# Optimization experiments

Measured on AMD Instinct MI355X. Metric: run time of the kernel, lower is better.

## Reference

```python
import jax, jax.numpy as jnp
import numpy as np

T, D_MODEL = 2048, 6144
NH, NKV, HD = 48, 8, 128
THETA, CAP = 10000.0, 30.0


def setup_inputs() -> dict:
    key = jax.random.key(0)
    k1, k2, k3 = jax.random.split(key, 3)
    return {
        "positions": jnp.arange(T, dtype=jnp.int32),
        "hidden_states": jax.random.normal(k1, (T, D_MODEL), jnp.float32),
        "w_qkv": jax.random.normal(k2, (D_MODEL, (NH + 2 * NKV) * HD), jnp.float32) * 0.02,
        "w_o": jax.random.normal(k3, (NH * HD, D_MODEL), jnp.float32) * 0.02,
    }


def _rope_neox(positions, x):
    # x: [T, h, HD]; neox-style: rotate concatenated halves
    half = HD // 2
    inv_freq = 1.0 / (THETA ** (jnp.arange(0, HD, 2, dtype=jnp.float32) / HD))  # [half]
    freqs = positions.astype(jnp.float32)[:, None] * inv_freq  # [T, half]
    cos = jnp.cos(freqs)[:, None, :]  # [T,1,half]
    sin = jnp.sin(freqs)[:, None, :]
    x1, x2 = x[..., :half], x[..., half:]
    return jnp.concatenate([x1 * cos - x2 * sin, x2 * cos + x1 * sin], axis=-1)


def reference(positions, hidden_states, w_qkv, w_o):
    qkv = hidden_states @ w_qkv  # [T, (NH+2*NKV)*HD]
    q, k, v = jnp.split(qkv, [NH * HD, NH * HD + NKV * HD], axis=-1)
    q = q.reshape(T, NH, HD)
    k = k.reshape(T, NKV, HD)
    v = v.reshape(T, NKV, HD)
    q = _rope_neox(positions, q)
    k = _rope_neox(positions, k)
    # GQA: expand kv heads to query heads
    g = NH // NKV
    k = jnp.repeat(k, g, axis=1)  # [T, NH, HD]
    v = jnp.repeat(v, g, axis=1)
    scale = HD ** -0.5
    logits = jnp.einsum('thd,shd->hts', q, k) * scale  # [NH, T, T]
    logits = CAP * jnp.tanh(logits / CAP)  # tanh logit softcapping
    causal = positions[:, None] >= positions[None, :]  # [T, T]
    logits = jnp.where(causal[None, :, :], logits, -jnp.inf)
    probs = jax.nn.softmax(logits, axis=-1)
    out = jnp.einsum('hts,shd->thd', probs, v)  # [T, NH, HD]
    out = out.reshape(T, NH * HD)
    return out @ w_o
```

## Files before the change

### kernel.cpp

```cpp
#include <hip/hip_runtime.h>
#include <hip/hip_bf16.h>
#include <stdint.h>

#define TSEQ   2048
#define DMODEL 6144
#define NHEADS 48
#define NKVH   8
#define HDIM   128
#define QKVC   8192
#define GRP    6

typedef __attribute__((ext_vector_type(8))) short short8;
typedef __attribute__((ext_vector_type(4))) float f32x4;


__device__ __forceinline__ unsigned short f2b(float f) {
  union { float f; unsigned int u; } v; v.f = f;
  unsigned int u = v.u;
  unsigned int r = (u + 0x7FFFu + ((u >> 16) & 1u)) >> 16;
  return (unsigned short)r;
}

__device__ __forceinline__ float b2f(unsigned short s) {
  union { unsigned int u; float f; } v; v.u = ((unsigned int)s) << 16;
  return v.f;
}

#if __has_builtin(__builtin_amdgcn_exp2f)
#define EXP2(x) __builtin_amdgcn_exp2f(x)
#else
#define EXP2(x) exp2f(x)
#endif
#if __has_builtin(__builtin_amdgcn_rcpf)
#define RCP(x) __builtin_amdgcn_rcpf(x)
#else
#define RCP(x) (1.0f / (x))
#endif

typedef const __attribute__((address_space(1))) void* as1_cvp;
typedef __attribute__((address_space(3))) void* as3_vp;

__device__ __forceinline__ void gload_lds16(const void* g, void* l) {
  __builtin_amdgcn_global_load_lds(
      (as1_cvp)(uintptr_t)g,
      (as3_vp)(unsigned int)(uintptr_t)l, 16, 0, 0);
}

#define LGKMC(n) do { asm volatile("s_waitcnt lgkmcnt(" #n ")" ::: "memory"); \
                      __builtin_amdgcn_sched_barrier(0); } while (0)
#define VMC(n) do { asm volatile("s_waitcnt vmcnt(" #n ")" ::: "memory"); \
                    __builtin_amdgcn_sched_barrier(0); } while (0)
#define BARR  do { asm volatile("s_barrier" ::: "memory"); } while (0)


__global__ __launch_bounds__(256) void k_cvt(const float* __restrict__ in,
                                             unsigned short* __restrict__ outp, int n) {
  int i = (blockIdx.x * 256 + threadIdx.x) * 8;
  if (i + 7 < n) {
    float4 va = *(const float4*)(in + i);
    float4 vb = *(const float4*)(in + i + 4);
    union { unsigned short s[8]; uint4 u; } o;
    o.s[0] = f2b(va.x); o.s[1] = f2b(va.y); o.s[2] = f2b(va.z); o.s[3] = f2b(va.w);
    o.s[4] = f2b(vb.x); o.s[5] = f2b(vb.y); o.s[6] = f2b(vb.z); o.s[7] = f2b(vb.w);
    *(uint4*)(outp + i) = o.u;
  }
}

__global__ __launch_bounds__(256) void k_tr2(const float* __restrict__ in, long istr, long zin,
                                             unsigned short* __restrict__ out, long ostr, long zout) {
  __shared__ unsigned short tile[64][68];
  const int tid = threadIdx.x;
  const int br = blockIdx.y * 64;
  const int bc = blockIdx.x * 64;
  in  += (size_t)blockIdx.z * zin;
  out += (size_t)blockIdx.z * zout;
  const int row = tid >> 4;
  const int c4  = (tid & 15) * 4;
#pragma unroll
  for (int p = 0; p < 4; ++p) {
    const int r = p * 16 + row;
    float4 v = *(const float4*)(in + (size_t)(br + r) * istr + bc + c4);
    tile[r][c4 + 0] = f2b(v.x);
    tile[r][c4 + 1] = f2b(v.y);
    tile[r][c4 + 2] = f2b(v.z);
    tile[r][c4 + 3] = f2b(v.w);
  }
  __syncthreads();
#pragma unroll
  for (int p = 0; p < 4; ++p) {
    const int r = p * 16 + row;
    union { unsigned short s[4]; uint2 u; } o;
    o.s[0] = tile[c4 + 0][r];
    o.s[1] = tile[c4 + 1][r];
    o.s[2] = tile[c4 + 2][r];
    o.s[3] = tile[c4 + 3][r];
    *(uint2*)(out + (size_t)(bc + r) * ostr + br + c4) = o.u;
  }
}

__global__ __launch_bounds__(256) void k_tr2b(const unsigned short* __restrict__ in, long istr, long zin,
                                              unsigned short* __restrict__ out, long ostr, long zout) {
  __shared__ unsigned short tile[64][68];
  const int tid = threadIdx.x;
  const int br = blockIdx.y * 64;
  const int bc = blockIdx.x * 64;
  in  += (size_t)blockIdx.z * zin;
  out += (size_t)blockIdx.z * zout;
  const int row = tid >> 4;
  const int c4  = (tid & 15) * 4;
#pragma unroll
  for (int p = 0; p < 4; ++p) {
    const int r = p * 16 + row;
    union { unsigned short s[4]; uint2 u; } v;
    v.u = *(const uint2*)(in + (size_t)(br + r) * istr + bc + c4);
    tile[r][c4 + 0] = v.s[0];
    tile[r][c4 + 1] = v.s[1];
    tile[r][c4 + 2] = v.s[2];
    tile[r][c4 + 3] = v.s[3];
  }
  __syncthreads();
#pragma unroll
  for (int p = 0; p < 4; ++p) {
    const int r = p * 16 + row;
    union { unsigned short s[4]; uint2 u; } o;
    o.s[0] = tile[c4 + 0][r];
    o.s[1] = tile[c4 + 1][r];
    o.s[2] = tile[c4 + 2][r];
    o.s[3] = tile[c4 + 3][r];
    *(uint2*)(out + (size_t)(bc + r) * ostr + br + c4) = o.u;
  }
}

__global__ void k_trig(const int* __restrict__ pos, float* __restrict__ cs,
                       float* __restrict__ sn) {
  int t = blockIdx.x, i = threadIdx.x;
  float p = (float)pos[t];
  float inv = EXP2(-(float)(2 * i) * (1.0f / 128.0f) * 13.287712379549449f);
  float f = p * inv;
  cs[t * 64 + i] = cosf(f);
  sn[t * 64 + i] = sinf(f);
}


#define READ_A(mh, aa) do { \
  _Pragma("unroll") for (int m = 0; m < 4; ++m) \
  _Pragma("unroll") for (int ks = 0; ks < 2; ++ks) \
    aa[m][ks] = *(const short8*)(LA + (wm * 128 + (mh) * 64 + m * 16 + lr) * 128 \
                                 + ((ks * 64 + lkb) ^ lsw)); } while (0)

#define READ_BR(s, cnt, bb) do { \
  _Pragma("unroll") for (int n2 = (s); n2 < (s) + (cnt); ++n2) \
  _Pragma("unroll") for (int ks = 0; ks < 2; ++ks) \
    bb[n2][ks] = *(const short8*)(LB + (wn * (16 * NH2) + n2 * 16 + lr) * 128 \
                                  + ((ks * 64 + lkb) ^ lsw)); } while (0)

#define CLUSTER(mh, s, cnt, aa, bb) do { \
  __builtin_amdgcn_s_setprio(1); \
  _Pragma("unroll") for (int m = 0; m < 4; ++m) \
  _Pragma("unroll") for (int n2 = (s); n2 < (s) + (cnt); ++n2) \
  _Pragma("unroll") for (int ks = 0; ks < 2; ++ks) \
    acc[(mh) * 4 + m][n2] = __builtin_amdgcn_mfma_f32_16x16x32_bf16( \
        aa[m][ks], bb[n2][ks], acc[(mh) * 4 + m][n2], 0, 0, 0); \
  __builtin_amdgcn_s_setprio(0); } while (0)

#define STAGE_A(kt, bb) do { \
  _Pragma("unroll") for (int i = 0; i < 4; ++i) \
    gload_lds16(Asrc + (size_t)(kt) * 64 + (size_t)i * 64 * K, \
                lds + (bb) * BUFSZ + F + i * 8192); } while (0)

#define STAGE_B(kt, bb) do { \
  _Pragma("unroll") for (int i = 0; i < NH2; ++i) \
    gload_lds16(Bsrc + (size_t)(kt) * 64 + (size_t)i * 64 * K, \
                lds + (bb) * BUFSZ + 32768 + F + i * 8192); } while (0)

template <int NH2, typename OutT>
__global__ __launch_bounds__(512, 2) void k_gemm8(const unsigned short* __restrict__ A,
                                                  const unsigned short* __restrict__ Bt,
                                                  OutT* __restrict__ C,
                                                  int M, int N, int K) {
  extern __shared__ __align__(16) unsigned char lds[];
  constexpr int BN    = 64 * NH2;
  constexpr int NB0   = (NH2 == 4) ? 2 : 1;
  constexpr int NB1   = NH2 - NB0;
  constexpr int BUFSZ = 32768 + NH2 * 8192;
  const int tid  = threadIdx.x;
  const int lane = tid & 63;
  const int wave = tid >> 6;
  const int wm = wave >> 2;
  const int wn = wave & 3;
  const int lr  = lane & 15;
  const int lkb = (lane >> 4) * 16;
  const int li4 = (lane >> 4) * 4;
  const int lsw = (lane & 7) << 4;

  const int mt = M >> 8;
  const int nt = N / BN;
  const int Cx = nt >> 3;
  const int lin = blockIdx.x;
  const int xcd = lin & 7;
  const int r   = lin >> 3;
  const int m0  = (r % mt) << 8;
  const int n0  = (xcd * Cx + r / mt) * BN;

  const int F   = tid * 16;
  const int r0  = F >> 7;
  const int cbs = (F & 127) ^ ((r0 & 7) << 4);
  const unsigned short* Asrc = A  + (size_t)(m0 + r0) * K + (cbs >> 1);
  const unsigned short* Bsrc = Bt + (size_t)(n0 + r0) * K + (cbs >> 1);

  const int NT = K >> 6;

  f32x4 acc[8][NH2];
#pragma unroll
  for (int i = 0; i < 8; ++i)
#pragma unroll
    for (int j = 0; j < NH2; ++j) acc[i][j] = (f32x4){0.f, 0.f, 0.f, 0.f};

  STAGE_A(0, 0);
  STAGE_B(0, 0);
  STAGE_A(1, 1);
  VMC(4);
  BARR;

  for (int t = 0; t < NT; ++t) {
    const int cur = t & 1;
    const unsigned char* LA = lds + cur * BUFSZ;
    const unsigned char* LB = LA + 32768;
    short8 a0[4][2], a1[4][2], b[NH2][2];

    READ_A(0, a0);
    READ_BR(0, NB0, b);
    if (t + 1 < NT) STAGE_B(t + 1, cur ^ 1);
    READ_BR(NB0, NB1, b);
    READ_A(1, a1);

    LGKMC(12);
    CLUSTER(0, 0, NB0, a0, b);
    LGKMC(8);
    CLUSTER(0, NB0, NB1, a0, b);
    LGKMC(0);
    CLUSTER(1, 0, NB0, a1, b);
    BARR;
    if (t + 2 < NT) STAGE_A(t + 2, cur);
    CLUSTER(1, NB0, NB1, a1, b);
    if (t + 2 < NT) { VMC(4); } else { VMC(0); }
    BARR;
  }

#pragma unroll
  for (int mh = 0; mh < 2; ++mh)
#pragma unroll
    for (int m = 0; m < 4; ++m)
#pragma unroll
      for (int n2 = 0; n2 < NH2; ++n2)
#pragma unroll
        for (int i = 0; i < 4; ++i) {
          int row = m0 + wm * 128 + mh * 64 + m * 16 + li4 + i;
          int col = n0 + wn * (16 * NH2) + n2 * 16 + lr;
          float v = acc[mh * 4 + m][n2][i];
          if constexpr (sizeof(OutT) == 2)
            C[(size_t)row * N + col] = (OutT)f2b(v);
          else
            C[(size_t)row * N + col] = (OutT)v;
        }
}


__global__ __launch_bounds__(256) void k_rope(const unsigned short* __restrict__ qkv,
                                              const float* __restrict__ cs,
                                              const float* __restrict__ sn,
                                              unsigned short* __restrict__ Q,
                                              unsigned short* __restrict__ K) {
  const int t = blockIdx.x;
  const int tid = threadIdx.x;
  const unsigned short* row = qkv + (size_t)t * QKVC;
  const float* c = cs + t * 64;
  const float* s = sn + t * 64;
  for (int p = tid; p < 56 * 16; p += 256) {
    const int h = p >> 4, q4 = (p & 15) * 4;
    const unsigned short* src = row + h * 128;
    union { unsigned short sh[4]; uint2 u; } x1u, x2u;
    x1u.u = *(const uint2*)(src + q4);
    x2u.u = *(const uint2*)(src + 64 + q4);
    float4 cc = *(const float4*)(c + q4);
    float4 ss = *(const float4*)(s + q4);
    unsigned short* dst = (h < NHEADS)
        ? Q + ((size_t)h * TSEQ + t) * HDIM
        : K + ((size_t)(h - NHEADS) * TSEQ + t) * HDIM;
    float x10 = b2f(x1u.sh[0]), x11 = b2f(x1u.sh[1]),
          x12 = b2f(x1u.sh[2]), x13 = b2f(x1u.sh[3]);
    float x20 = b2f(x2u.sh[0]), x21 = b2f(x2u.sh[1]),
          x22 = b2f(x2u.sh[2]), x23 = b2f(x2u.sh[3]);
    union { unsigned short sh[4]; uint2 u; } o1, o2;
    o1.sh[0] = f2b(x10 * cc.x - x20 * ss.x);
    o1.sh[1] = f2b(x11 * cc.y - x21 * ss.y);
    o1.sh[2] = f2b(x12 * cc.z - x22 * ss.z);
    o1.sh[3] = f2b(x13 * cc.w - x23 * ss.w);
    o2.sh[0] = f2b(x20 * cc.x + x10 * ss.x);
    o2.sh[1] = f2b(x21 * cc.y + x11 * ss.y);
    o2.sh[2] = f2b(x22 * cc.z + x12 * ss.z);
    o2.sh[3] = f2b(x23 * cc.w + x13 * ss.w);
    *(uint2*)(dst + q4) = o1.u;
    *(uint2*)(dst + 64 + q4) = o2.u;
  }
}


__global__ __launch_bounds__(256, 2) void k_attn3(const unsigned short* __restrict__ Q,
                                                  const unsigned short* __restrict__ K,
                                                  const unsigned short* __restrict__ V,
                                                  unsigned short* __restrict__ O) {
  __shared__ __align__(16) unsigned char KsB[2][16384];
  __shared__ __align__(16) unsigned char VsB[2][16384];
  __shared__ __align__(16) unsigned char PsB[4][2048];

  const int lin = blockIdx.x;
  const int g   = lin & 7;
  const int rr  = lin >> 3;
  const int hg  = rr % 6;
  const int pr  = rr / 6;
  const int h   = g * 6 + hg;
  const int tid = threadIdx.x, wave = tid >> 6, lane = tid & 63;
  const int lr = lane & 15, lk = (lane >> 4) * 8, li4 = (lane >> 4) * 4;
  const unsigned short* Qh = Q + (size_t)h * (TSEQ * HDIM);
  const unsigned char*  Kb = (const unsigned char*)(K + (size_t)g * (TSEQ * HDIM));
  const unsigned char*  Vb = (const unsigned char*)(V + (size_t)g * (TSEQ * HDIM));
  unsigned char* Pw = PsB[wave];

#define STAGE_KV(st_, b_) do { \
  const int s_ = (st_) * 64; \
  _Pragma("unroll") for (int c = 0; c < 4; ++c) { \
    const int FF = tid * 16 + c * 4096; \
    const int krow = FF >> 8; \
    const int kcol = (FF & 255) ^ ((krow & 7) << 4); \
    gload_lds16(Kb + (size_t)(s_ + krow) * 256 + kcol, KsB[b_] + FF); \
    const int vrow = FF >> 7; \
    const int vcol = (FF & 127) ^ ((vrow & 7) << 4); \
    gload_lds16(Vb + (size_t)vrow * (TSEQ * 2) + (size_t)s_ * 2 + vcol, VsB[b_] + FF); \
  } } while (0)

  for (int half = 0; half < 2; ++half) {
    const int j  = half ? (31 - pr) : pr;
    const int t0 = j * 64 + wave * 16;
    const int nst = j + 1;

    short8 qf[4];
#pragma unroll
    for (int ks = 0; ks < 4; ++ks)
      qf[ks] = *(const short8*)(Qh + (size_t)(t0 + lr) * HDIM + ks * 32 + lk);

    f32x4 oacc[8];
#pragma unroll
    for (int n = 0; n < 8; ++n) oacc[n] = (f32x4){0.f, 0.f, 0.f, 0.f};
    float rs4[4] = {0.f, 0.f, 0.f, 0.f};

    STAGE_KV(0, 0);
    VMC(0);
    BARR;

    for (int st = 0; st < nst; ++st) {
      const int cur = st & 1;
      if (st + 1 < nst) STAGE_KV(st + 1, cur ^ 1);

      const unsigned char* Ks = KsB[cur];
      const unsigned char* Vs = VsB[cur];
      const int s0 = st * 64;
      f32x4 sacc[4];
#pragma unroll
      for (int n = 0; n < 4; ++n) sacc[n] = (f32x4){0.f, 0.f, 0.f, 0.f};
#pragma unroll
      for (int ks = 0; ks < 4; ++ks) {
        short8 kf[4];
#pragma unroll
        for (int n = 0; n < 4; ++n) {
          const int row = n * 16 + lr;
          kf[n] = *(const short8*)(Ks + row * 256 + ((ks * 64 + lk * 2) ^ ((row & 7) << 4)));
        }
#pragma unroll
        for (int n = 0; n < 4; ++n)
          sacc[n] = __builtin_amdgcn_mfma_f32_16x16x32_bf16(qf[ks], kf[n], sacc[n], 0, 0, 0);
      }

      const bool lastst = (st == nst - 1);
#pragma unroll
      for (int n = 0; n < 4; ++n)
#pragma unroll
        for (int i = 0; i < 4; ++i) {
          float sv = sacc[n][i] * 0.08838834764831845f;
          float e = EXP2(sv * 0.09617966939259757f);
          float p = EXP2(-86.5617024533378f * RCP(e + 1.0f));
          if (lastst && (s0 + n * 16 + lr > t0 + li4 + i)) p = 0.f;
          rs4[i] += p;
          const int prow = li4 + i;
          *(unsigned short*)(Pw + prow * 128 +
              (((n * 16 + lr) * 2) ^ ((prow & 7) << 4))) = f2b(p);
        }

#pragma unroll
      for (int ks2 = 0; ks2 < 2; ++ks2) {
        short8 pf = *(const short8*)(Pw + lr * 128 +
                         (((ks2 * 32 + lk) * 2) ^ ((lr & 7) << 4)));
        short8 vf[8];
#pragma unroll
        for (int n = 0; n < 8; ++n) {
          const int row = n * 16 + lr;
          vf[n] = *(const short8*)(Vs + row * 128 + ((ks2 * 64 + lk * 2) ^ ((row & 7) << 4)));
        }
#pragma unroll
        for (int n = 0; n < 8; ++n)
          oacc[n] = __builtin_amdgcn_mfma_f32_16x16x32_bf16(pf, vf[n], oacc[n], 0, 0, 0);
      }

      VMC(0);
      BARR;
    }

    float inv4[4];
#pragma unroll
    for (int i = 0; i < 4; ++i) {
      float v = rs4[i];
      v += __shfl_xor(v, 1, 64);
      v += __shfl_xor(v, 2, 64);
      v += __shfl_xor(v, 4, 64);
      v += __shfl_xor(v, 8, 64);
      inv4[i] = RCP(v);
    }
#pragma unroll
    for (int n = 0; n < 8; ++n)
#pragma unroll
      for (int i = 0; i < 4; ++i)
        O[(size_t)(t0 + li4 + i) * DMODEL + h * HDIM + n * 16 + lr] =
            f2b(oacc[n][i] * inv4[i]);
    BARR;
  }
#undef STAGE_KV
}


extern "C" void kernel_launch(void* const* d_in, const int* in_sizes, int n_in,
                              void* d_out, int out_size, void* d_ws, size_t ws_size,
                              hipStream_t stream) {
  const int*   pos  = (const int*)d_in[0];
  const float* hid  = (const float*)d_in[1];
  const float* wqkv = (const float*)d_in[2];
  const float* wo   = (const float*)d_in[3];
  float* out = (float*)d_out;
  char* ws = (char*)d_ws;

  const size_t O_XB   = 0;
  const size_t O_WQT  = 25165824;
  const size_t O_WOT  = 125829120;
  const size_t O_QKV  = 201326592;
  const size_t O_TRIG = 268435456;

  unsigned short* Xb  = (unsigned short*)(ws + O_XB);
  unsigned short* Wqt = (unsigned short*)(ws + O_WQT);
  unsigned short* Wot = (unsigned short*)(ws + O_WOT);
  unsigned short* QKVb = (unsigned short*)(ws + O_QKV);
  float* CS  = (float*)(ws + O_TRIG);
  float* SN  = CS + TSEQ * 64;
  unsigned short* Qr = Wqt;
  unsigned short* Kr = Wqt + (size_t)NHEADS * TSEQ * HDIM;
  unsigned short* Vt = Kr + (size_t)NKVH * TSEQ * HDIM;
  unsigned short* AO = Xb;

  hipFuncSetAttribute((const void*)k_gemm8<4, unsigned short>,
                      hipFuncAttributeMaxDynamicSharedMemorySize, 131072);
  hipFuncSetAttribute((const void*)k_gemm8<3, float>,
                      hipFuncAttributeMaxDynamicSharedMemorySize, 114688);

  k_cvt<<<(TSEQ * DMODEL) / (256 * 8), 256, 0, stream>>>(hid, Xb, TSEQ * DMODEL);
  k_tr2<<<dim3(QKVC / 64, DMODEL / 64, 1), 256, 0, stream>>>(wqkv, QKVC, 0, Wqt, DMODEL, 0);
  k_tr2<<<dim3(DMODEL / 64, DMODEL / 64, 1), 256, 0, stream>>>(wo, DMODEL, 0, Wot, DMODEL, 0);
  k_trig<<<TSEQ, 64, 0, stream>>>(pos, CS, SN);

  k_gemm8<4, unsigned short><<<(TSEQ / 256) * (QKVC / 256), 512, 131072, stream>>>(
      Xb, Wqt, QKVb, TSEQ, QKVC, DMODEL);
  k_rope<<<TSEQ, 256, 0, stream>>>(QKVb, CS, SN, Qr, Kr);
  k_tr2b<<<dim3(HDIM / 64, TSEQ / 64, NKVH), 256, 0, stream>>>(
      QKVb + (size_t)(DMODEL + NKVH * HDIM), QKVC, HDIM,
      Vt, TSEQ, (size_t)HDIM * TSEQ);
  k_attn3<<<768, 256, 0, stream>>>(Qr, Kr, Vt, AO);
  k_gemm8<3, float><<<(TSEQ / 256) * (DMODEL / 192), 512, 114688, stream>>>(
      AO, Wot, out, TSEQ, DMODEL, DMODEL);
}
```

Baseline: 525.1 us.

## Double query rows per wave in attention to reuse K/V tiles

The attention kernel now handles 128 query rows per block (32 per wave, as two 16-row MFMA tiles) instead of 64, so each staged K/V tile in shared memory feeds twice as many MFMAs. The grid drops from 768 to 384 blocks, the P buffer grows, and causal masking now covers the last two KV stages. This cuts redundant K/V global loads and LDS reads per unit of work. The cost is higher register pressure (two sets of accumulators), fewer blocks for load balance across CUs, and extra work on fully masked tiles in the diagonal stages.

```diff
diff --git a/kernel.cpp b/kernel.cpp
--- a/kernel.cpp
+++ b/kernel.cpp
@@ -306,13 +306,13 @@
 }
 
 
-__global__ __launch_bounds__(256, 2) void k_attn3(const unsigned short* __restrict__ Q,
+__global__ __launch_bounds__(256, 2) void k_attn4(const unsigned short* __restrict__ Q,
                                                   const unsigned short* __restrict__ K,
                                                   const unsigned short* __restrict__ V,
                                                   unsigned short* __restrict__ O) {
   __shared__ __align__(16) unsigned char KsB[2][16384];
   __shared__ __align__(16) unsigned char VsB[2][16384];
-  __shared__ __align__(16) unsigned char PsB[4][2048];
+  __shared__ __align__(16) unsigned char PsB[4][4096];
 
   const int lin = blockIdx.x;
   const int g   = lin & 7;
@@ -340,19 +340,23 @@
   } } while (0)
 
   for (int half = 0; half < 2; ++half) {
-    const int j  = half ? (31 - pr) : pr;
-    const int t0 = j * 64 + wave * 16;
-    const int nst = j + 1;
-
-    short8 qf[4];
-#pragma unroll
-    for (int ks = 0; ks < 4; ++ks)
-      qf[ks] = *(const short8*)(Qh + (size_t)(t0 + lr) * HDIM + ks * 32 + lk);
-
-    f32x4 oacc[8];
-#pragma unroll
-    for (int n = 0; n < 8; ++n) oacc[n] = (f32x4){0.f, 0.f, 0.f, 0.f};
-    float rs4[4] = {0.f, 0.f, 0.f, 0.f};
+    const int j  = half ? (15 - pr) : pr;
+    const int t0 = j * 128 + wave * 32;
+    const int nst = 2 * (j + 1);
+
+    short8 qf[2][4];
+#pragma unroll
+    for (int m = 0; m < 2; ++m)
+#pragma unroll
+      for (int ks = 0; ks < 4; ++ks)
+        qf[m][ks] = *(const short8*)(Qh + (size_t)(t0 + m * 16 + lr) * HDIM + ks * 32 + lk);
+
+    f32x4 oacc[2][8];
+#pragma unroll
+    for (int m = 0; m < 2; ++m)
+#pragma unroll
+      for (int n = 0; n < 8; ++n) oacc[m][n] = (f32x4){0.f, 0.f, 0.f, 0.f};
+    float rs4[2][4] = {{0.f, 0.f, 0.f, 0.f}, {0.f, 0.f, 0.f, 0.f}};
 
     STAGE_KV(0, 0);
     VMC(0);
@@ -365,9 +369,12 @@
       const unsigned char* Ks = KsB[cur];
       const unsigned char* Vs = VsB[cur];
       const int s0 = st * 64;
-      f32x4 sacc[4];
-#pragma unroll
-      for (int n = 0; n < 4; ++n) sacc[n] = (f32x4){0.f, 0.f, 0.f, 0.f};
+
+      f32x4 sacc[2][4];
+#pragma unroll
+      for (int m = 0; m < 2; ++m)
+#pragma unroll
+        for (int n = 0; n < 4; ++n) sacc[m][n] = (f32x4){0.f, 0.f, 0.f, 0.f};
 #pragma unroll
       for (int ks = 0; ks < 4; ++ks) {
         short8 kf[4];
@@ -377,29 +384,38 @@
           kf[n] = *(const short8*)(Ks + row * 256 + ((ks * 64 + lk * 2) ^ ((row & 7) << 4)));
         }
 #pragma unroll
+        for (int m = 0; m < 2; ++m)
+#pragma unroll
+          for (int n = 0; n < 4; ++n)
+            sacc[m][n] = __builtin_amdgcn_mfma_f32_16x16x32_bf16(qf[m][ks], kf[n], sacc[m][n], 0, 0, 0);
+      }
+
+      const bool maskst = (st >= nst - 2);
+#pragma unroll
+      for (int m = 0; m < 2; ++m)
+#pragma unroll
         for (int n = 0; n < 4; ++n)
-          sacc[n] = __builtin_amdgcn_mfma_f32_16x16x32_bf16(qf[ks], kf[n], sacc[n], 0, 0, 0);
-      }
-
-      const bool lastst = (st == nst - 1);
-#pragma unroll
-      for (int n = 0; n < 4; ++n)
-#pragma unroll
-        for (int i = 0; i < 4; ++i) {
-          float sv = sacc[n][i] * 0.08838834764831845f;
-          float e = EXP2(sv * 0.09617966939259757f);
-          float p = EXP2(-86.5617024533378f * RCP(e + 1.0f));
-          if (lastst && (s0 + n * 16 + lr > t0 + li4 + i)) p = 0.f;
-          rs4[i] += p;
-          const int prow = li4 + i;
-          *(unsigned short*)(Pw + prow * 128 +
-              (((n * 16 + lr) * 2) ^ ((prow & 7) << 4))) = f2b(p);
+#pragma unroll
+          for (int i = 0; i < 4; ++i) {
+            float e = EXP2(sacc[m][n][i] *
+                           (0.08838834764831845f * 0.09617966939259757f));
+            float p = EXP2(-86.5617024533378f * RCP(e + 1.0f));
+            if (maskst && (s0 + n * 16 + lr > t0 + m * 16 + li4 + i)) p = 0.f;
+            rs4[m][i] += p;
+            const int prow = m * 16 + li4 + i;
+            *(unsigned short*)(Pw + prow * 128 +
+                (((n * 16 + lr) * 2) ^ ((prow & 7) << 4))) = f2b(p);
+          }
+
+#pragma unroll
+      for (int ks2 = 0; ks2 < 2; ++ks2) {
+        short8 pf[2];
+#pragma unroll
+        for (int m = 0; m < 2; ++m) {
+          const int prow = m * 16 + lr;
+          pf[m] = *(const short8*)(Pw + prow * 128 +
+                       (((ks2 * 32 + lk) * 2) ^ ((prow & 7) << 4)));
         }
-
-#pragma unroll
-      for (int ks2 = 0; ks2 < 2; ++ks2) {
-        short8 pf = *(const short8*)(Pw + lr * 128 +
-                         (((ks2 * 32 + lk) * 2) ^ ((lr & 7) << 4)));
         short8 vf[8];
 #pragma unroll
         for (int n = 0; n < 8; ++n) {
@@ -407,30 +423,35 @@
           vf[n] = *(const short8*)(Vs + row * 128 + ((ks2 * 64 + lk * 2) ^ ((row & 7) << 4)));
         }
 #pragma unroll
-        for (int n = 0; n < 8; ++n)
-          oacc[n] = __builtin_amdgcn_mfma_f32_16x16x32_bf16(pf, vf[n], oacc[n], 0, 0, 0);
+        for (int m = 0; m < 2; ++m)
+#pragma unroll
+          for (int n = 0; n < 8; ++n)
+            oacc[m][n] = __builtin_amdgcn_mfma_f32_16x16x32_bf16(pf[m], vf[n], oacc[m][n], 0, 0, 0);
       }
 
       VMC(0);
       BARR;
     }
 
-    float inv4[4];
-#pragma unroll
-    for (int i = 0; i < 4; ++i) {
-      float v = rs4[i];
-      v += __shfl_xor(v, 1, 64);
-      v += __shfl_xor(v, 2, 64);
-      v += __shfl_xor(v, 4, 64);
-      v += __shfl_xor(v, 8, 64);
-      inv4[i] = RCP(v);
+#pragma unroll
+    for (int m = 0; m < 2; ++m) {
+      float inv4[4];
+#pragma unroll
+      for (int i = 0; i < 4; ++i) {
+        float v = rs4[m][i];
+        v += __shfl_xor(v, 1, 64);
+        v += __shfl_xor(v, 2, 64);
+        v += __shfl_xor(v, 4, 64);
+        v += __shfl_xor(v, 8, 64);
+        inv4[i] = RCP(v);
+      }
+#pragma unroll
+      for (int n = 0; n < 8; ++n)
+#pragma unroll
+        for (int i = 0; i < 4; ++i)
+          O[(size_t)(t0 + m * 16 + li4 + i) * DMODEL + h * HDIM + n * 16 + lr] =
+              f2b(oacc[m][n][i] * inv4[i]);
     }
-#pragma unroll
-    for (int n = 0; n < 8; ++n)
-#pragma unroll
-      for (int i = 0; i < 4; ++i)
-        O[(size_t)(t0 + li4 + i) * DMODEL + h * HDIM + n * 16 + lr] =
-            f2b(oacc[n][i] * inv4[i]);
     BARR;
   }
 #undef STAGE_KV
@@ -480,7 +501,7 @@
   k_tr2b<<<dim3(HDIM / 64, TSEQ / 64, NKVH), 256, 0, stream>>>(
       QKVb + (size_t)(DMODEL + NKVH * HDIM), QKVC, HDIM,
       Vt, TSEQ, (size_t)HDIM * TSEQ);
-  k_attn3<<<768, 256, 0, stream>>>(Qr, Kr, Vt, AO);
+  k_attn4<<<384, 256, 0, stream>>>(Qr, Kr, Vt, AO);
   k_gemm8<3, float><<<(TSEQ / 256) * (DMODEL / 192), 512, 114688, stream>>>(
       AO, Wot, out, TSEQ, DMODEL, DMODEL);
 }
```

Measured after the change: 536.4 us. 2.1% more time.
